# Optimization experiments

Hardware: AMD Instinct MI355X
Metric: run time of the kernel (lower is better)

## Reference

```python
import jax, jax.numpy as jnp
import numpy as np
import math

B, S, D, H = 8, 2048, 1024, 16
DH = D // H  # attention head size = 64

def setup_inputs() -> dict:
    key = jax.random.key(0)
    ks = jax.random.split(key, 10)
    s = 1.0 / math.sqrt(D)
    return {
        "hidden_states": jax.random.normal(ks[0], (B, S, D), dtype=jnp.float32),
        "attention_mask": jnp.zeros((B, 1, S), dtype=jnp.float32),
        "Wq": jax.random.normal(ks[1], (D, D), dtype=jnp.float32) * s,
        "bq": jnp.zeros((D,), dtype=jnp.float32),
        "Wqa": jax.random.normal(ks[2], (D, H), dtype=jnp.float32) * s,
        "bqa": jnp.zeros((H,), dtype=jnp.float32),
        "Wk": jax.random.normal(ks[3], (D, D), dtype=jnp.float32) * s,
        "bk": jnp.zeros((D,), dtype=jnp.float32),
        "Wt": jax.random.normal(ks[4], (D, D), dtype=jnp.float32) * s,
        "bt": jnp.zeros((D,), dtype=jnp.float32),
    }

def reference(hidden_states, attention_mask, Wq, bq, Wqa, bqa, Wk, bk, Wt, bt):
    scale = 1.0 / math.sqrt(DH)
    q = hidden_states @ Wq + bq                      # [B,S,D] mixed_query_layer
    k = hidden_states @ Wk + bk                      # [B,S,D] mixed_key_layer
    # query attention logits -> [B,H,S]
    q_score = jnp.swapaxes(q @ Wqa + bqa, 1, 2) * scale + attention_mask
    q_weight = jax.nn.softmax(q_score, axis=-1)      # [B,H,S]
    ql = jnp.swapaxes(q.reshape(B, S, H, DH), 1, 2)  # [B,H,S,DH]
    kl = jnp.swapaxes(k.reshape(B, S, H, DH), 1, 2)  # [B,H,S,DH]
    pooled_q = jnp.einsum('bhs,bhsd->bhd', q_weight, ql)          # [B,H,DH]
    qk_score = jnp.einsum('bhsd,bhd->bhs', kl, pooled_q) * scale + attention_mask
    qk_weight = jax.nn.softmax(qk_score, axis=-1)                 # [B,H,S]
    pooled_k = jnp.einsum('bhs,bhsd->bhd', qk_weight, kl)         # [B,H,DH]
    weighted = pooled_k[:, :, None, :] * ql                       # [B,H,S,DH]
    weighted = jnp.swapaxes(weighted, 1, 2).reshape(B, S, D)      # [B,S,D]
    out = weighted @ Wt + bt + q                                  # transform + residual to query
    return out
```

## Files before the change

### kernel.cpp

```cpp
#include <hip/hip_runtime.h>
#include <hip/hip_bf16.h>
#include <math.h>

#define BB 8
#define SS 2048
#define DD 1024
#define HH 16
#define DHH 64
#define NROWS (BB*SS)
#define QSLICE ((size_t)BB * HH * SS)

typedef unsigned short u16;
typedef __attribute__((ext_vector_type(8))) __bf16 bf16x8;
typedef __attribute__((ext_vector_type(4))) float f32x4;

__device__ __forceinline__ u16 f2bf(float f) {
    union { float f; unsigned u; } v; v.f = f;
    unsigned r = v.u + 0x7fffu + ((v.u >> 16) & 1u);
    return (u16)(r >> 16);
}
__device__ __forceinline__ float bf2f(u16 b) {
    union { unsigned u; float f; } v; v.u = ((unsigned)b) << 16;
    return v.f;
}

__device__ __forceinline__ void load_lds16(const void* g, void* l) {
    __builtin_amdgcn_global_load_lds(
        (const __attribute__((address_space(1))) unsigned int*)g,
        (__attribute__((address_space(3))) unsigned int*)l,
        16, 0, 0);
}

__global__ __launch_bounds__(256) void cast_bf16_kernel(const float* __restrict__ in,
                                                        u16* __restrict__ out, int n4) {
    int i = blockIdx.x * 256 + threadIdx.x;
    if (i >= n4) return;
    float4 v = ((const float4*)in)[i];
    ushort4 o;
    o.x = f2bf(v.x); o.y = f2bf(v.y); o.z = f2bf(v.z); o.w = f2bf(v.w);
    ((ushort4*)out)[i] = o;
}

__global__ __launch_bounds__(256) void transpose_cast_kernel(const float* __restrict__ W,
                                                             u16* __restrict__ WT) {
    __shared__ float tile[32][33];
    int m0 = blockIdx.x * 32, k0 = blockIdx.y * 32;
    int tx = threadIdx.x & 31, ty = threadIdx.x >> 5;
    #pragma unroll
    for (int i = 0; i < 4; i++) {
        int kk = ty + i * 8;
        tile[kk][tx] = W[(k0 + kk) * DD + m0 + tx];
    }
    __syncthreads();
    #pragma unroll
    for (int i = 0; i < 4; i++) {
        int mm = ty + i * 8;
        WT[(m0 + mm) * DD + k0 + tx] = f2bf(tile[tx][mm]);
    }
}

__global__ __launch_bounds__(256) void wqa_transpose_kernel(const float* __restrict__ Wqa,
                                                            u16* __restrict__ WqaT) {
    int i = blockIdx.x * 256 + threadIdx.x;
    int h = i >> 10, k = i & 1023;
    WqaT[i] = f2bf(Wqa[k * HH + h]);
}

template<int MODE>
__global__ __launch_bounds__(256)
void gemm_kernel(const u16* __restrict__ A, const u16* __restrict__ BT,
                 const float* __restrict__ bias, const u16* __restrict__ res,
                 float* __restrict__ Cf, u16* __restrict__ Cb) {
    __shared__ u16 sA[128 * 64];
    __shared__ u16 sB[128 * 64];
    const int row0 = blockIdx.x * 128;
    const int col0 = blockIdx.y * 128;
    const int t = threadIdx.x;
    const int w = t >> 6, lane = t & 63;
    const int wr = (w >> 1) * 64, wc = (w & 1) * 64;
    const int m16 = lane & 15, quad = lane >> 4;

    f32x4 acc[4][4];
    #pragma unroll
    for (int i = 0; i < 4; i++)
        #pragma unroll
        for (int j = 0; j < 4; j++)
            acc[i][j] = (f32x4){0.f, 0.f, 0.f, 0.f};

    const int srow = t >> 3;
    const int scol = ((t & 7) ^ (srow & 7)) * 8;
    const u16* Ag = A + (size_t)(row0 + srow) * DD + scol;
    const u16* Bg = BT + (size_t)(col0 + srow) * DD + scol;

    for (int k0 = 0; k0 < DD; k0 += 64) {
        __syncthreads();
        #pragma unroll
        for (int j = 0; j < 4; j++) {
            load_lds16(Ag + k0 + (size_t)j * 32 * DD, &sA[j * 2048 + t * 8]);
            load_lds16(Bg + k0 + (size_t)j * 32 * DD, &sB[j * 2048 + t * 8]);
        }
        __syncthreads();
        #pragma unroll
        for (int ks = 0; ks < 2; ks++) {
            const int cpos = ((ks * 4 + quad) ^ (m16 & 7)) * 8;
            bf16x8 af[4], bfr[4];
            #pragma unroll
            for (int i = 0; i < 4; i++) {
                af[i]  = *(const bf16x8*)&sA[(wr + i * 16 + m16) * 64 + cpos];
                bfr[i] = *(const bf16x8*)&sB[(wc + i * 16 + m16) * 64 + cpos];
            }
            #pragma unroll
            for (int mi = 0; mi < 4; mi++)
                #pragma unroll
                for (int ni = 0; ni < 4; ni++)
                    acc[mi][ni] = __builtin_amdgcn_mfma_f32_16x16x32_bf16(
                        af[mi], bfr[ni], acc[mi][ni], 0, 0, 0);
        }
    }

    #pragma unroll
    for (int mi = 0; mi < 4; mi++) {
        #pragma unroll
        for (int r = 0; r < 4; r++) {
            int row = row0 + wr + mi * 16 + quad * 4 + r;
            #pragma unroll
            for (int ni = 0; ni < 4; ni++) {
                int col = col0 + wc + ni * 16 + m16;
                float v = acc[mi][ni][r] + bias[col];
                size_t idx = (size_t)row * DD + col;
                if (MODE == 1) Cb[idx] = f2bf(v);
                else Cf[idx] = v + bf2f(res[idx]);
            }
        }
    }
}

__global__ __launch_bounds__(256)
void qscore_mfma_kernel(const u16* __restrict__ qbf, const u16* __restrict__ WqaT,
                        float* __restrict__ qraw) {
    int w = threadIdx.x >> 6, lane = threadIdx.x & 63;
    int row0 = blockIdx.x * 64 + w * 16;
    int kbase = blockIdx.y * 256;
    int m16 = lane & 15, quad = lane >> 4;
    f32x4 acc = (f32x4){0.f, 0.f, 0.f, 0.f};
    const u16* ap = qbf + (size_t)(row0 + m16) * DD + kbase + quad * 8;
    const u16* bp = WqaT + (size_t)m16 * DD + kbase + quad * 8;
    #pragma unroll
    for (int kk = 0; kk < 256; kk += 32) {
        bf16x8 a = *(const bf16x8*)(ap + kk);
        bf16x8 b = *(const bf16x8*)(bp + kk);
        acc = __builtin_amdgcn_mfma_f32_16x16x32_bf16(a, b, acc, 0, 0, 0);
    }
    #pragma unroll
    for (int r = 0; r < 4; r++) {
        int grow = row0 + quad * 4 + r;
        int b = grow >> 11, sidx = grow & 2047;
        qraw[((size_t)(blockIdx.y * BB + b) * HH + m16) * SS + sidx] = acc[r];
    }
}

template<bool EPI>
__global__ __launch_bounds__(256)
void softmax_kernel(float* __restrict__ score, const float* __restrict__ bqa,
                    const float* __restrict__ mask) {
    int bh = blockIdx.x;
    int b = bh >> 4, h = bh & 15;
    float* srow = score + ((size_t)bh << 11);
    __shared__ float rm[4], rs[4];
    int t = threadIdx.x;

    float v[8];
    float m = -1e30f;
    #pragma unroll
    for (int i = 0; i < 8; i++) {
        int off = t + i * 256;
        float x;
        if (EPI) {
            x = srow[off] + srow[off + QSLICE] + srow[off + 2 * QSLICE] + srow[off + 3 * QSLICE];
            x = (x + bqa[h]) * 0.125f + mask[b * SS + off];
        } else {
            x = srow[off];
        }
        v[i] = x; m = fmaxf(m, x);
    }
    #pragma unroll
    for (int off = 32; off; off >>= 1) m = fmaxf(m, __shfl_xor(m, off));
    if ((t & 63) == 0) rm[t >> 6] = m;
    __syncthreads();
    m = fmaxf(fmaxf(rm[0], rm[1]), fmaxf(rm[2], rm[3]));

    float sum = 0.f;
    #pragma unroll
    for (int i = 0; i < 8; i++) { v[i] = __expf(v[i] - m); sum += v[i]; }
    #pragma unroll
    for (int off = 32; off; off >>= 1) sum += __shfl_xor(sum, off);
    if ((t & 63) == 0) rs[t >> 6] = sum;
    __syncthreads();
    float inv = 1.0f / (rs[0] + rs[1] + rs[2] + rs[3]);
    #pragma unroll
    for (int i = 0; i < 8; i++) srow[t + i * 256] = v[i] * inv;
}

__global__ __launch_bounds__(256)
void pool_kernel(const float* __restrict__ w, const u16* __restrict__ X,
                 float* __restrict__ pooled) {
    int b = blockIdx.x;
    int s0 = blockIdx.y * 32;
    int t = threadIdx.x;
    int wid = t >> 6, lane = t & 63;
    int h = lane >> 2;
    __shared__ float sw[16 * 33];
    __shared__ float pr[4][64 * 17];
    {
        int hh = t >> 4, si = t & 15;
        const float* wr = w + ((size_t)(b * HH + hh) << 11) + s0;
        sw[hh * 33 + si] = wr[si];
        sw[hh * 33 + si + 16] = wr[si + 16];
    }
    __syncthreads();
    float acc[16];
    #pragma unroll
    for (int j = 0; j < 16; j++) acc[j] = 0.f;
    const u16* xbase = X + ((size_t)(b * SS + s0 + wid * 8) << 10) + lane * 16;
    #pragma unroll
    for (int rr = 0; rr < 8; rr++) {
        float ws = sw[h * 33 + wid * 8 + rr];
        const uint4* xp = (const uint4*)(xbase + (size_t)rr * DD);
        uint4 x0 = xp[0], x1 = xp[1];
        unsigned xw[8] = {x0.x, x0.y, x0.z, x0.w, x1.x, x1.y, x1.z, x1.w};
        #pragma unroll
        for (int i2 = 0; i2 < 8; i2++) {
            union { unsigned u; float f; } lo, hi;
            lo.u = xw[i2] << 16; hi.u = xw[i2] & 0xffff0000u;
            acc[2 * i2]     += ws * lo.f;
            acc[2 * i2 + 1] += ws * hi.f;
        }
    }
    #pragma unroll
    for (int j = 0; j < 16; j++) pr[wid][lane * 17 + j] = acc[j];
    __syncthreads();
    #pragma unroll
    for (int i = 0; i < 4; i++) {
        int idx = t + i * 256;
        int l2 = idx >> 4, j2 = idx & 15;
        float v = pr[0][l2 * 17 + j2] + pr[1][l2 * 17 + j2] +
                  pr[2][l2 * 17 + j2] + pr[3][l2 * 17 + j2];
        int od = (l2 >> 2) * 64 + (l2 & 3) * 16 + j2;
        atomicAdd(&pooled[b * DD + od], v);
    }
}

__global__ __launch_bounds__(256)
void qkscore_kernel(const u16* __restrict__ kbf, const float* __restrict__ pq,
                    const float* __restrict__ mask, float* __restrict__ qkscore) {
    int row = blockIdx.x * 4 + (threadIdx.x >> 6);
    int lane = threadIdx.x & 63;
    int b = row >> 11, s = row & 2047;
    int h = lane >> 2, dp = lane & 3;
    const u16* kp = kbf + (size_t)row * DD + h * 64 + dp * 16;
    const float* pqp = pq + (size_t)(b * HH + h) * 64 + dp * 16;
    const uint4* kp4 = (const uint4*)kp;
    uint4 ka = kp4[0], kb4 = kp4[1];
    unsigned kw[8] = {ka.x, ka.y, ka.z, ka.w, kb4.x, kb4.y, kb4.z, kb4.w};
    float acc = 0.f;
    #pragma unroll
    for (int i = 0; i < 8; i++) {
        union { unsigned u; float f; } lo, hi;
        lo.u = kw[i] << 16;
        hi.u = kw[i] & 0xffff0000u;
        acc += lo.f * pqp[2 * i] + hi.f * pqp[2 * i + 1];
    }
    acc += __shfl_xor(acc, 1);
    acc += __shfl_xor(acc, 2);
    if (dp == 0) qkscore[(size_t)(b * HH + h) * SS + s] = acc * 0.125f + mask[b * SS + s];
}

__global__ __launch_bounds__(256)
void weighted_kernel(const u16* __restrict__ qbf, const float* __restrict__ pk,
                     u16* __restrict__ wout) {
    int i = blockIdx.x * 256 + threadIdx.x;
    int row = i >> 8;
    int c0 = (i & 255) << 2;
    int b = row >> 11;
    int h = c0 >> 6, d = c0 & 63;
    ushort4 qv = ((const ushort4*)qbf)[i];
    const float4 pv = *(const float4*)(pk + (size_t)(b * HH + h) * 64 + d);
    ushort4 o;
    o.x = f2bf(bf2f(qv.x) * pv.x); o.y = f2bf(bf2f(qv.y) * pv.y);
    o.z = f2bf(bf2f(qv.z) * pv.z); o.w = f2bf(bf2f(qv.w) * pv.w);
    ((ushort4*)wout)[i] = o;
}

extern "C" void kernel_launch(void* const* d_in, const int* in_sizes, int n_in,
                              void* d_out, int out_size, void* d_ws, size_t ws_size,
                              hipStream_t stream) {
    const float* hs   = (const float*)d_in[0];
    const float* mask = (const float*)d_in[1];
    const float* Wq   = (const float*)d_in[2];
    const float* bq   = (const float*)d_in[3];
    const float* Wqa  = (const float*)d_in[4];
    const float* bqa  = (const float*)d_in[5];
    const float* Wk   = (const float*)d_in[6];
    const float* bk   = (const float*)d_in[7];
    const float* Wt   = (const float*)d_in[8];
    const float* bt   = (const float*)d_in[9];
    float* out = (float*)d_out;

    char* ws = (char*)d_ws;
    u16*   hs_bf = (u16*)ws;   ws += (size_t)NROWS * DD * 2;
    u16*   WqT   = (u16*)ws;   ws += (size_t)DD * DD * 2;
    u16*   WkT   = (u16*)ws;   ws += (size_t)DD * DD * 2;
    u16*   WtT   = (u16*)ws;   ws += (size_t)DD * DD * 2;
    u16*   WqaT  = (u16*)ws;   ws += (size_t)HH * DD * 2;
    u16*   q_bf  = (u16*)ws;   ws += (size_t)NROWS * DD * 2;
    u16*   k_bf  = (u16*)ws;   ws += (size_t)NROWS * DD * 2;
    float* qraw  = (float*)ws; ws += QSLICE * 4 * 4;
    float* qksc  = (float*)ws; ws += (size_t)BB * HH * SS * 4;
    float* pq    = (float*)ws; ws += (size_t)BB * HH * 64 * 4;
    float* pk    = (float*)ws; ws += (size_t)BB * HH * 64 * 4;
    u16*   wbf   = hs_bf;

    int n4 = NROWS * DD / 4;
    cast_bf16_kernel<<<n4 / 256, 256, 0, stream>>>(hs, hs_bf, n4);
    transpose_cast_kernel<<<dim3(32, 32), 256, 0, stream>>>(Wq, WqT);
    transpose_cast_kernel<<<dim3(32, 32), 256, 0, stream>>>(Wk, WkT);
    transpose_cast_kernel<<<dim3(32, 32), 256, 0, stream>>>(Wt, WtT);
    wqa_transpose_kernel<<<HH * DD / 256, 256, 0, stream>>>(Wqa, WqaT);

    hipMemsetAsync(pq, 0, (size_t)BB * HH * 64 * 4, stream);
    hipMemsetAsync(pk, 0, (size_t)BB * HH * 64 * 4, stream);

    gemm_kernel<1><<<dim3(NROWS / 128, DD / 128), 256, 0, stream>>>(hs_bf, WqT, bq, nullptr, nullptr, q_bf);
    gemm_kernel<1><<<dim3(NROWS / 128, DD / 128), 256, 0, stream>>>(hs_bf, WkT, bk, nullptr, nullptr, k_bf);

    qscore_mfma_kernel<<<dim3(NROWS / 64, 4), 256, 0, stream>>>(q_bf, WqaT, qraw);
    softmax_kernel<true><<<BB * HH, 256, 0, stream>>>(qraw, bqa, mask);
    pool_kernel<<<dim3(BB, SS / 32), 256, 0, stream>>>(qraw, q_bf, pq);
    qkscore_kernel<<<NROWS / 4, 256, 0, stream>>>(k_bf, pq, mask, qksc);
    softmax_kernel<false><<<BB * HH, 256, 0, stream>>>(qksc, nullptr, nullptr);
    pool_kernel<<<dim3(BB, SS / 32), 256, 0, stream>>>(qksc, k_bf, pk);
    weighted_kernel<<<n4 / 256, 256, 0, stream>>>(q_bf, pk, wbf);

    gemm_kernel<2><<<dim3(NROWS / 128, DD / 128), 256, 0, stream>>>(wbf, WtT, bt, q_bf, out, nullptr);
}
```

Before: 330.7 us.

## Fold pooled_k scaling into per-batch Wt and use 32x32 MFMA GEMMs

Instead of forming weighted = q * pooled_k over all rows, the per-batch scale is folded into a per-batch copy of the transposed Wt, so the output GEMM reads q directly. This removes a full activation pass over B*S*D. The Q and K projections are also merged into one launch, and the GEMM core moves from 16x16x32 to 32x32x16 MFMA tiles. In exchange it writes B scaled copies of Wt (16 MB of bf16), and pq/pk buffers are resized to B*D.

Result: no change. 332.3 us (+0.5%).

```diff
diff --git a/kernel.cpp b/kernel.cpp
--- a/kernel.cpp
+++ b/kernel.cpp
@@ -13,6 +13,7 @@
 typedef unsigned short u16;
 typedef __attribute__((ext_vector_type(8))) __bf16 bf16x8;
 typedef __attribute__((ext_vector_type(4))) float f32x4;
+typedef __attribute__((ext_vector_type(16))) float f32x16;
 
 __device__ __forceinline__ u16 f2bf(float f) {
     union { float f; unsigned u; } v; v.f = f;
@@ -66,73 +67,122 @@
     WqaT[i] = f2bf(Wqa[k * HH + h]);
 }
 
-template<int MODE>
-__global__ __launch_bounds__(256)
-void gemm_kernel(const u16* __restrict__ A, const u16* __restrict__ BT,
-                 const float* __restrict__ bias, const u16* __restrict__ res,
-                 float* __restrict__ Cf, u16* __restrict__ Cb) {
+__device__ __forceinline__ void gemm_core(const u16* __restrict__ A,
+                                          const u16* __restrict__ BT,
+                                          int row0, int col0,
+                                          u16* sA, u16* sB,
+                                          f32x16 acc[2][2]) {
+    const int t = threadIdx.x;
+    const int lane = t & 63;
+    const int w = t >> 6;
+    const int wr = (w >> 1) * 64, wc = (w & 1) * 64;
+    const int l31 = lane & 31, khalf = lane >> 5;
+
+    #pragma unroll
+    for (int i = 0; i < 2; i++)
+        #pragma unroll
+        for (int j = 0; j < 2; j++)
+            #pragma unroll
+            for (int r = 0; r < 16; r++)
+                acc[i][j][r] = 0.f;
+
+    const int srow = t >> 3;
+    const int scol = ((t & 7) ^ (srow & 7)) * 8;
+    const u16* Ag = A + (size_t)(row0 + srow) * DD + scol;
+    const u16* Bg = BT + (size_t)(col0 + srow) * DD + scol;
+
+    for (int k0 = 0; k0 < DD; k0 += 64) {
+        __syncthreads();
+        #pragma unroll
+        for (int j = 0; j < 4; j++) {
+            load_lds16(Ag + k0 + (size_t)j * 32 * DD, &sA[j * 2048 + t * 8]);
+            load_lds16(Bg + k0 + (size_t)j * 32 * DD, &sB[j * 2048 + t * 8]);
+        }
+        __syncthreads();
+        #pragma unroll
+        for (int ks = 0; ks < 4; ks++) {
+            const int cpos = ((ks * 2 + khalf) ^ (l31 & 7)) * 8;
+            bf16x8 af[2], bfr[2];
+            #pragma unroll
+            for (int i = 0; i < 2; i++) {
+                af[i]  = *(const bf16x8*)&sA[(wr + i * 32 + l31) * 64 + cpos];
+                bfr[i] = *(const bf16x8*)&sB[(wc + i * 32 + l31) * 64 + cpos];
+            }
+            #pragma unroll
+            for (int mi = 0; mi < 2; mi++)
+                #pragma unroll
+                for (int ni = 0; ni < 2; ni++)
+                    acc[mi][ni] = __builtin_amdgcn_mfma_f32_32x32x16_bf16(
+                        af[mi], bfr[ni], acc[mi][ni], 0, 0, 0);
+        }
+    }
+}
+
+__global__ __launch_bounds__(256)
+void gemm_qk_kernel(const u16* __restrict__ A,
+                    const u16* __restrict__ WqT, const u16* __restrict__ WkT,
+                    const float* __restrict__ bq, const float* __restrict__ bk,
+                    u16* __restrict__ qb, u16* __restrict__ kb) {
+    __shared__ u16 sA[128 * 64];
+    __shared__ u16 sB[128 * 64];
+    const int row0 = blockIdx.x * 128;
+    const bool isQ = blockIdx.y < 8;
+    const int col0 = (isQ ? blockIdx.y : blockIdx.y - 8) * 128;
+    const u16* BT = isQ ? WqT : WkT;
+    const float* bias = isQ ? bq : bk;
+    u16* Cb = isQ ? qb : kb;
+
+    f32x16 acc[2][2];
+    gemm_core(A, BT, row0, col0, sA, sB, acc);
+
+    const int lane = threadIdx.x & 63, w = threadIdx.x >> 6;
+    const int wr = (w >> 1) * 64, wc = (w & 1) * 64;
+    const int l31 = lane & 31, khalf = lane >> 5;
+    #pragma unroll
+    for (int ti = 0; ti < 2; ti++)
+        #pragma unroll
+        for (int tj = 0; tj < 2; tj++) {
+            int col = col0 + wc + tj * 32 + l31;
+            float bv = bias[col];
+            #pragma unroll
+            for (int r = 0; r < 16; r++) {
+                int m = (r & 3) + 8 * (r >> 2) + 4 * khalf;
+                int row = row0 + wr + ti * 32 + m;
+                Cb[(size_t)row * DD + col] = f2bf(acc[ti][tj][r] + bv);
+            }
+        }
+}
+
+__global__ __launch_bounds__(256)
+void gemm_out_kernel(const u16* __restrict__ A, const u16* __restrict__ WtTs,
+                     const float* __restrict__ bt, const u16* __restrict__ res,
+                     float* __restrict__ out) {
     __shared__ u16 sA[128 * 64];
     __shared__ u16 sB[128 * 64];
     const int row0 = blockIdx.x * 128;
     const int col0 = blockIdx.y * 128;
-    const int t = threadIdx.x;
-    const int w = t >> 6, lane = t & 63;
+    const u16* BT = WtTs + (size_t)(row0 >> 11) * DD * DD;
+
+    f32x16 acc[2][2];
+    gemm_core(A, BT, row0, col0, sA, sB, acc);
+
+    const int lane = threadIdx.x & 63, w = threadIdx.x >> 6;
     const int wr = (w >> 1) * 64, wc = (w & 1) * 64;
-    const int m16 = lane & 15, quad = lane >> 4;
-
-    f32x4 acc[4][4];
-    #pragma unroll
-    for (int i = 0; i < 4; i++)
-        #pragma unroll
-        for (int j = 0; j < 4; j++)
-            acc[i][j] = (f32x4){0.f, 0.f, 0.f, 0.f};
-
-    const int srow = t >> 3;
-    const int scol = ((t & 7) ^ (srow & 7)) * 8;
-    const u16* Ag = A + (size_t)(row0 + srow) * DD + scol;
-    const u16* Bg = BT + (size_t)(col0 + srow) * DD + scol;
-
-    for (int k0 = 0; k0 < DD; k0 += 64) {
-        __syncthreads();
-        #pragma unroll
-        for (int j = 0; j < 4; j++) {
-            load_lds16(Ag + k0 + (size_t)j * 32 * DD, &sA[j * 2048 + t * 8]);
-            load_lds16(Bg + k0 + (size_t)j * 32 * DD, &sB[j * 2048 + t * 8]);
-        }
-        __syncthreads();
-        #pragma unroll
-        for (int ks = 0; ks < 2; ks++) {
-            const int cpos = ((ks * 4 + quad) ^ (m16 & 7)) * 8;
-            bf16x8 af[4], bfr[4];
-            #pragma unroll
-            for (int i = 0; i < 4; i++) {
-                af[i]  = *(const bf16x8*)&sA[(wr + i * 16 + m16) * 64 + cpos];
-                bfr[i] = *(const bf16x8*)&sB[(wc + i * 16 + m16) * 64 + cpos];
+    const int l31 = lane & 31, khalf = lane >> 5;
+    #pragma unroll
+    for (int ti = 0; ti < 2; ti++)
+        #pragma unroll
+        for (int tj = 0; tj < 2; tj++) {
+            int col = col0 + wc + tj * 32 + l31;
+            float bv = bt[col];
+            #pragma unroll
+            for (int r = 0; r < 16; r++) {
+                int m = (r & 3) + 8 * (r >> 2) + 4 * khalf;
+                int row = row0 + wr + ti * 32 + m;
+                size_t idx = (size_t)row * DD + col;
+                out[idx] = acc[ti][tj][r] + bv + bf2f(res[idx]);
             }
-            #pragma unroll
-            for (int mi = 0; mi < 4; mi++)
-                #pragma unroll
-                for (int ni = 0; ni < 4; ni++)
-                    acc[mi][ni] = __builtin_amdgcn_mfma_f32_16x16x32_bf16(
-                        af[mi], bfr[ni], acc[mi][ni], 0, 0, 0);
-        }
-    }
-
-    #pragma unroll
-    for (int mi = 0; mi < 4; mi++) {
-        #pragma unroll
-        for (int r = 0; r < 4; r++) {
-            int row = row0 + wr + mi * 16 + quad * 4 + r;
-            #pragma unroll
-            for (int ni = 0; ni < 4; ni++) {
-                int col = col0 + wc + ni * 16 + m16;
-                float v = acc[mi][ni][r] + bias[col];
-                size_t idx = (size_t)row * DD + col;
-                if (MODE == 1) Cb[idx] = f2bf(v);
-                else Cf[idx] = v + bf2f(res[idx]);
-            }
-        }
-    }
+        }
 }
 
 __global__ __launch_bounds__(256)
@@ -276,19 +326,18 @@
 }
 
 __global__ __launch_bounds__(256)
-void weighted_kernel(const u16* __restrict__ qbf, const float* __restrict__ pk,
-                     u16* __restrict__ wout) {
+void scale_wt_kernel(const u16* __restrict__ WtT, const float* __restrict__ pk,
+                     u16* __restrict__ WtTs) {
     int i = blockIdx.x * 256 + threadIdx.x;
-    int row = i >> 8;
-    int c0 = (i & 255) << 2;
-    int b = row >> 11;
-    int h = c0 >> 6, d = c0 & 63;
-    ushort4 qv = ((const ushort4*)qbf)[i];
-    const float4 pv = *(const float4*)(pk + (size_t)(b * HH + h) * 64 + d);
+    int b = i >> 18;
+    int m = (i >> 8) & 1023;
+    int k4 = (i & 255) << 2;
+    ushort4 wv = ((const ushort4*)WtT)[(m << 8) + (i & 255)];
+    const float4 p = *(const float4*)(pk + b * DD + k4);
     ushort4 o;
-    o.x = f2bf(bf2f(qv.x) * pv.x); o.y = f2bf(bf2f(qv.y) * pv.y);
-    o.z = f2bf(bf2f(qv.z) * pv.z); o.w = f2bf(bf2f(qv.w) * pv.w);
-    ((ushort4*)wout)[i] = o;
+    o.x = f2bf(bf2f(wv.x) * p.x); o.y = f2bf(bf2f(wv.y) * p.y);
+    o.z = f2bf(bf2f(wv.z) * p.z); o.w = f2bf(bf2f(wv.w) * p.w);
+    ((ushort4*)WtTs)[i] = o;
 }
 
 extern "C" void kernel_launch(void* const* d_in, const int* in_sizes, int n_in,
@@ -316,9 +365,9 @@
     u16*   k_bf  = (u16*)ws;   ws += (size_t)NROWS * DD * 2;
     float* qraw  = (float*)ws; ws += QSLICE * 4 * 4;
     float* qksc  = (float*)ws; ws += (size_t)BB * HH * SS * 4;
-    float* pq    = (float*)ws; ws += (size_t)BB * HH * 64 * 4;
-    float* pk    = (float*)ws; ws += (size_t)BB * HH * 64 * 4;
-    u16*   wbf   = hs_bf;
+    float* pq    = (float*)ws; ws += (size_t)BB * DD * 4;
+    float* pk    = (float*)ws; ws += (size_t)BB * DD * 4;
+    u16*   WtTs  = (u16*)ws;   ws += (size_t)BB * DD * DD * 2;
 
     int n4 = NROWS * DD / 4;
     cast_bf16_kernel<<<n4 / 256, 256, 0, stream>>>(hs, hs_bf, n4);
@@ -327,11 +376,10 @@
     transpose_cast_kernel<<<dim3(32, 32), 256, 0, stream>>>(Wt, WtT);
     wqa_transpose_kernel<<<HH * DD / 256, 256, 0, stream>>>(Wqa, WqaT);
 
-    hipMemsetAsync(pq, 0, (size_t)BB * HH * 64 * 4, stream);
-    hipMemsetAsync(pk, 0, (size_t)BB * HH * 64 * 4, stream);
-
-    gemm_kernel<1><<<dim3(NROWS / 128, DD / 128), 256, 0, stream>>>(hs_bf, WqT, bq, nullptr, nullptr, q_bf);
-    gemm_kernel<1><<<dim3(NROWS / 128, DD / 128), 256, 0, stream>>>(hs_bf, WkT, bk, nullptr, nullptr, k_bf);
+    hipMemsetAsync(pq, 0, (size_t)BB * DD * 4, stream);
+    hipMemsetAsync(pk, 0, (size_t)BB * DD * 4, stream);
+
+    gemm_qk_kernel<<<dim3(NROWS / 128, 16), 256, 0, stream>>>(hs_bf, WqT, WkT, bq, bk, q_bf, k_bf);
 
     qscore_mfma_kernel<<<dim3(NROWS / 64, 4), 256, 0, stream>>>(q_bf, WqaT, qraw);
     softmax_kernel<true><<<BB * HH, 256, 0, stream>>>(qraw, bqa, mask);
@@ -339,7 +387,7 @@
     qkscore_kernel<<<NROWS / 4, 256, 0, stream>>>(k_bf, pq, mask, qksc);
     softmax_kernel<false><<<BB * HH, 256, 0, stream>>>(qksc, nullptr, nullptr);
     pool_kernel<<<dim3(BB, SS / 32), 256, 0, stream>>>(qksc, k_bf, pk);
-    weighted_kernel<<<n4 / 256, 256, 0, stream>>>(q_bf, pk, wbf);
-
-    gemm_kernel<2><<<dim3(NROWS / 128, DD / 128), 256, 0, stream>>>(wbf, WtT, bt, q_bf, out, nullptr);
-}
+
+    scale_wt_kernel<<<(BB * DD * DD / 4) / 256, 256, 0, stream>>>(WtT, pk, WtTs);
+    gemm_out_kernel<<<dim3(NROWS / 128, DD / 128), 256, 0, stream>>>(q_bf, WtTs, bt, q_bf, out);
+}
```
